# Optimization experiments

Measured on AMD Instinct MI355X. Metric: run time of the kernel, lower is better.

The kernel has to match this reference:

```python
import jax, jax.numpy as jnp
import numpy as np

NEG_SLOPE = 0.2  # PyG GATConv default leaky_relu slope
EPS = 1e-16


def layer_norm(x, g, b):
    mu = x.mean(-1, keepdims=True)
    var = ((x - mu) ** 2).mean(-1, keepdims=True)
    return (x - mu) * jax.lax.rsqrt(var + 1e-5) * g + b


def gat_conv(x, src, dst, n, W, a_src, a_dst, bias):
    # x: [N, C_in]; W: [C_in, H*C]; a_src/a_dst: [H, C]; concat=False -> mean over heads
    H, C = a_src.shape
    xh = (x @ W).reshape(n, H, C)                      # [N, H, C]
    s_src = jnp.einsum('nhc,hc->nh', xh, a_src)         # [N, H]
    s_dst = jnp.einsum('nhc,hc->nh', xh, a_dst)         # [N, H]
    e = jax.nn.leaky_relu(s_src[src] + s_dst[dst], NEG_SLOPE)  # [E, H]
    # segment softmax over incoming edges of each destination node
    m = jax.ops.segment_max(e, dst, num_segments=n)     # [N, H]
    ee = jnp.exp(e - m[dst])
    z = jax.ops.segment_sum(ee, dst, num_segments=n)    # [N, H]
    alpha = ee / (z[dst] + EPS)                         # [E, H]
    msg = xh[src] * alpha[:, :, None]                   # [E, H, C]
    out = jax.ops.segment_sum(msg, dst, num_segments=n) # [N, H, C]
    return out.mean(axis=1) + bias                      # [N, C]


def setup_inputs() -> dict:
    key = jax.random.key(0)
    N, E, C, H, L = 50000, 400000, 64, 4, 2
    ks = jax.random.split(key, 16)
    x = jax.random.normal(ks[0], (N, C), dtype=jnp.float32)
    edge_index = jax.random.randint(ks[1], (2, E), 0, N, dtype=jnp.int64)
    sc = 1.0 / np.sqrt(C)
    return {
        'x': x,
        'edge_index': edge_index,
        'Wg': jax.random.normal(ks[2], (L, C, H * C), dtype=jnp.float32) * sc,
        'att_src': jax.random.normal(ks[3], (L, H, C), dtype=jnp.float32) * sc,
        'att_dst': jax.random.normal(ks[4], (L, H, C), dtype=jnp.float32) * sc,
        'att_bias': jnp.zeros((L, C), dtype=jnp.float32),
        'ln1_g': jnp.ones((L, C), dtype=jnp.float32),
        'ln1_b': jnp.zeros((L, C), dtype=jnp.float32),
        'W1': jax.random.normal(ks[5], (L, C, C), dtype=jnp.float32) * sc,
        'b1': jnp.zeros((L, C), dtype=jnp.float32),
        'W2': jax.random.normal(ks[6], (L, C, C), dtype=jnp.float32) * sc,
        'b2': jnp.zeros((L, C), dtype=jnp.float32),
        'ln2_g': jnp.ones((L, C), dtype=jnp.float32),
        'ln2_b': jnp.zeros((L, C), dtype=jnp.float32),
    }


def reference(x, edge_index, Wg, att_src, att_dst, att_bias,
              ln1_g, ln1_b, W1, b1, W2, b2, ln2_g, ln2_b):
    n = x.shape[0]
    L = Wg.shape[0]
    # PyG GATConv adds self loops by default
    loops = jnp.arange(n, dtype=edge_index.dtype)
    src = jnp.concatenate([edge_index[0], loops])
    dst = jnp.concatenate([edge_index[1], loops])
    for i in range(L):
        x_att = gat_conv(x, src, dst, n, Wg[i], att_src[i], att_dst[i], att_bias[i])
        x = layer_norm(x + x_att, ln1_g[i], ln1_b[i])
        h = jax.nn.relu(x @ W1[i] + b1[i])
        h = h @ W2[i] + b2[i]
        x = layer_norm(x + h, ln2_g[i], ln2_b[i])
    return x
```

## Files before the change

kernel.cpp:

```cpp
#include <hip/hip_runtime.h>
#include <hip/hip_bf16.h>
#include <float.h>

#define C 64
#define H 4
#define HC 256
#define NEG_SLOPE 0.2f
#define EPS_SEG 1e-16f
#define LN_EPS 1e-5f

typedef __attribute__((ext_vector_type(8))) short bf16x8;
typedef __attribute__((ext_vector_type(4))) float f32x4;

__device__ __forceinline__ float warp_sum(float v) {
#pragma unroll
    for (int m = 32; m >= 1; m >>= 1) v += __shfl_xor(v, m, 64);
    return v;
}

__device__ __forceinline__ unsigned short f2bf(float f) {
    unsigned int u = __float_as_uint(f);
    return (unsigned short)((u + 0x7FFF + ((u >> 16) & 1)) >> 16);
}
__device__ __forceinline__ float bf2f(unsigned short u) {
    return __uint_as_float(((unsigned int)u) << 16);
}


__global__ void k_zero(int* __restrict__ a, int n) {
    int i = blockIdx.x * blockDim.x + threadIdx.x;
    int stride = gridDim.x * blockDim.x;
    for (int j = i; j < n; j += stride) a[j] = 0;
}

__global__ void k_count(const int* __restrict__ ei, int* __restrict__ counts,
                        int E, int Etot) {
    int eid = blockIdx.x * blockDim.x + threadIdx.x;
    if (eid >= Etot) return;
    int d = (eid < E) ? ei[E + eid] : eid - E;
    atomicAdd(&counts[d], 1);
}

__global__ __launch_bounds__(256) void k_scan1(const int* __restrict__ counts,
                                               int* __restrict__ tmp,
                                               int* __restrict__ bsum, int N) {
    __shared__ int sm[256];
    int t = threadIdx.x;
    int i = blockIdx.x * 256 + t;
    sm[t] = (i < N) ? counts[i] : 0;
    __syncthreads();
    for (int off = 1; off < 256; off <<= 1) {
        int add = (t >= off) ? sm[t - off] : 0;
        __syncthreads();
        sm[t] += add;
        __syncthreads();
    }
    if (i < N) tmp[i] = sm[t];
    if (t == 255) bsum[blockIdx.x] = sm[255];
}

__global__ __launch_bounds__(256) void k_scan2(int* __restrict__ bsum, int nb) {
    __shared__ int sm[256];
    int t = threadIdx.x;
    sm[t] = (t < nb) ? bsum[t] : 0;
    __syncthreads();
    for (int off = 1; off < 256; off <<= 1) {
        int add = (t >= off) ? sm[t - off] : 0;
        __syncthreads();
        sm[t] += add;
        __syncthreads();
    }
    if (t < nb) bsum[t] = (t > 0) ? sm[t - 1] : 0;
}

__global__ __launch_bounds__(256) void k_scan3(const int* __restrict__ tmp,
                                               const int* __restrict__ boff,
                                               int* __restrict__ rowptr,
                                               int* __restrict__ cursor, int N) {
    int i = blockIdx.x * 256 + threadIdx.x;
    if (i < N) {
        rowptr[i + 1] = tmp[i] + boff[blockIdx.x];
        cursor[i] = 0;
    }
    if (i == 0) rowptr[0] = 0;
}

__global__ void k_fill(const int* __restrict__ ei, const int* __restrict__ rowptr,
                       int* __restrict__ cursor, int* __restrict__ col,
                       int* __restrict__ dcol, int E, int Etot) {
    int eid = blockIdx.x * blockDim.x + threadIdx.x;
    if (eid >= Etot) return;
    int s, d;
    if (eid < E) { s = ei[eid]; d = ei[E + eid]; } else { s = d = eid - E; }
    int pos = rowptr[d] + atomicAdd(&cursor[d], 1);
    col[pos] = s;
    dcol[pos] = d;
}


__global__ void k_prep_x(const float4* __restrict__ xin, ushort4* __restrict__ xb,
                         int n4, int npad4) {
    int i = blockIdx.x * blockDim.x + threadIdx.x;
    int st = gridDim.x * blockDim.x;
    for (int j = i; j < npad4; j += st) {
        ushort4 o;
        if (j < n4) {
            float4 v = xin[j];
            o.x = f2bf(v.x); o.y = f2bf(v.y); o.z = f2bf(v.z); o.w = f2bf(v.w);
        } else {
            o.x = o.y = o.z = o.w = 0;
        }
        xb[j] = o;
    }
}

__global__ void k_prep_w(const float* __restrict__ Wg, unsigned short* __restrict__ Wgt,
                         int L) {
    int i = blockIdx.x * 256 + threadIdx.x;
    if (i < L * C * HC) {
        int l = i / (C * HC);
        int r = i - l * C * HC;
        int n = r >> 6, k = r & 63;
        Wgt[(size_t)l * HC * C + n * C + k] = f2bf(Wg[(size_t)l * C * HC + k * HC + n]);
    }
}

__global__ void k_prep_fw(const float* __restrict__ W1, const float* __restrict__ W2,
                          unsigned short* __restrict__ W1t, unsigned short* __restrict__ W2t,
                          int L) {
    int i = blockIdx.x * 256 + threadIdx.x;
    if (i < L * C * C) {
        int l = i / (C * C);
        int r = i - l * C * C;
        int n = r >> 6, k = r & 63;
        W1t[(size_t)l * C * C + n * C + k] = f2bf(W1[(size_t)l * C * C + k * C + n]);
        W2t[(size_t)l * C * C + n * C + k] = f2bf(W2[(size_t)l * C * C + k * C + n]);
    }
}

__global__ __launch_bounds__(256) void k_gemm_mfma(
    const unsigned short* __restrict__ xb, const unsigned short* __restrict__ Wgt,
    const float* __restrict__ a_src, const float* __restrict__ a_dst,
    unsigned short* __restrict__ xh, float* __restrict__ s_src,
    float* __restrict__ s_dst, int N)
{
    int w = threadIdx.x >> 6, l = threadIdx.x & 63;
    int n0 = blockIdx.x * 64;
    int lr = l & 15, lk = (l >> 4) * 8;
    bf16x8 bfr[4][2];
    float as[4], ad[4];
#pragma unroll
    for (int ct = 0; ct < 4; ct++) {
        int colg = w * 64 + ct * 16 + lr;
#pragma unroll
        for (int ks = 0; ks < 2; ks++)
            bfr[ct][ks] = *reinterpret_cast<const bf16x8*>(Wgt + colg * C + ks * 32 + lk);
        as[ct] = a_src[w * C + ct * 16 + lr];
        ad[ct] = a_dst[w * C + ct * 16 + lr];
    }
#pragma unroll
    for (int rt = 0; rt < 4; rt++) {
        const unsigned short* arow = xb + (size_t)(n0 + rt * 16 + lr) * C + lk;
        bf16x8 a0 = *reinterpret_cast<const bf16x8*>(arow);
        bf16x8 a1 = *reinterpret_cast<const bf16x8*>(arow + 32);
        f32x4 acc[4];
#pragma unroll
        for (int ct = 0; ct < 4; ct++) {
            acc[ct] = (f32x4){0.f, 0.f, 0.f, 0.f};
            acc[ct] = __builtin_amdgcn_mfma_f32_16x16x32_bf16(a0, bfr[ct][0], acc[ct], 0, 0, 0);
            acc[ct] = __builtin_amdgcn_mfma_f32_16x16x32_bf16(a1, bfr[ct][1], acc[ct], 0, 0, 0);
        }
        int nbase = n0 + rt * 16 + (l >> 4) * 4;
#pragma unroll
        for (int ct = 0; ct < 4; ct++) {
            int colg = w * 64 + ct * 16 + lr;
#pragma unroll
            for (int r = 0; r < 4; r++) {
                int n = nbase + r;
                if (n < N) xh[(size_t)n * HC + colg] = f2bf(acc[ct][r]);
            }
        }
#pragma unroll
        for (int r = 0; r < 4; r++) {
            float ps = acc[0][r] * as[0] + acc[1][r] * as[1]
                     + acc[2][r] * as[2] + acc[3][r] * as[3];
            float pd = acc[0][r] * ad[0] + acc[1][r] * ad[1]
                     + acc[2][r] * ad[2] + acc[3][r] * ad[3];
#pragma unroll
            for (int off = 1; off < 16; off <<= 1) {
                ps += __shfl_xor(ps, off, 64);
                pd += __shfl_xor(pd, off, 64);
            }
            int n = nbase + r;
            if (lr == 0 && n < N) {
                s_src[n * H + w] = ps;
                s_dst[n * H + w] = pd;
            }
        }
    }
}

__global__ void k_edge_w(const int* __restrict__ col, const int* __restrict__ dcol,
                         const float* __restrict__ s_src, const float* __restrict__ s_dst,
                         float* __restrict__ wbuf, int Etot) {
    int i = blockIdx.x * blockDim.x + threadIdx.x;
    if (i >= Etot * H) return;
    int p = i >> 2, h = i & 3;
    int s = col[p], d = dcol[p];
    float e = s_src[s * H + h] + s_dst[d * H + h];
    e = e >= 0.f ? e : NEG_SLOPE * e;
    wbuf[i] = __expf(e);
}

__global__ __launch_bounds__(256) void k_gat_node(
    const int* __restrict__ rowptr, const int* __restrict__ col,
    const float* __restrict__ wbuf, const unsigned short* __restrict__ xh,
    const float* __restrict__ x_in, const float* __restrict__ bias,
    const float* __restrict__ g, const float* __restrict__ b,
    float* __restrict__ x1, unsigned short* __restrict__ x1b, int N)
{
    int n = (blockIdx.x * blockDim.x + threadIdx.x) >> 6;
    int l = threadIdx.x & 63;
    int h = l >> 4, gq = l & 15;
    if (n >= N) return;
    int r0 = rowptr[n], r1 = rowptr[n + 1];

    float4 xi = *(const float4*)(x_in + (size_t)n * C + gq * 4);
    float4 bia = *(const float4*)(bias + gq * 4);

    const char* xbase = (const char*)xh;
    int laneoff = h * 128 + gq * 8;

    float a0 = 0.f, a1 = 0.f, a2 = 0.f, a3 = 0.f, z = 0.f;

    int j = r0;
    for (; j + 4 <= r1; j += 4) {
        int s0 = col[j], s1 = col[j + 1], s2 = col[j + 2], s3 = col[j + 3];
        float w0 = wbuf[(j + 0) * H + h];
        float w1 = wbuf[(j + 1) * H + h];
        float w2 = wbuf[(j + 2) * H + h];
        float w3 = wbuf[(j + 3) * H + h];
        uint2 v0 = *(const uint2*)(xbase + (size_t)s0 * 512 + laneoff);
        uint2 v1 = *(const uint2*)(xbase + (size_t)s1 * 512 + laneoff);
        uint2 v2 = *(const uint2*)(xbase + (size_t)s2 * 512 + laneoff);
        uint2 v3 = *(const uint2*)(xbase + (size_t)s3 * 512 + laneoff);
        a0 += w0 * __uint_as_float(v0.x << 16);
        a1 += w0 * __uint_as_float(v0.x & 0xFFFF0000u);
        a2 += w0 * __uint_as_float(v0.y << 16);
        a3 += w0 * __uint_as_float(v0.y & 0xFFFF0000u);
        a0 += w1 * __uint_as_float(v1.x << 16);
        a1 += w1 * __uint_as_float(v1.x & 0xFFFF0000u);
        a2 += w1 * __uint_as_float(v1.y << 16);
        a3 += w1 * __uint_as_float(v1.y & 0xFFFF0000u);
        a0 += w2 * __uint_as_float(v2.x << 16);
        a1 += w2 * __uint_as_float(v2.x & 0xFFFF0000u);
        a2 += w2 * __uint_as_float(v2.y << 16);
        a3 += w2 * __uint_as_float(v2.y & 0xFFFF0000u);
        a0 += w3 * __uint_as_float(v3.x << 16);
        a1 += w3 * __uint_as_float(v3.x & 0xFFFF0000u);
        a2 += w3 * __uint_as_float(v3.y << 16);
        a3 += w3 * __uint_as_float(v3.y & 0xFFFF0000u);
        z += w0 + w1 + w2 + w3;
    }
    {
        int t = r1 - j;
        int s0 = 0, s1 = 0, s2 = 0;
        float w0 = 0.f, w1 = 0.f, w2 = 0.f;
        if (t > 0) { s0 = col[j];     w0 = wbuf[(j + 0) * H + h]; }
        if (t > 1) { s1 = col[j + 1]; w1 = wbuf[(j + 1) * H + h]; }
        if (t > 2) { s2 = col[j + 2]; w2 = wbuf[(j + 2) * H + h]; }
        uint2 v0 = {0, 0}, v1 = {0, 0}, v2 = {0, 0};
        if (t > 0) v0 = *(const uint2*)(xbase + (size_t)s0 * 512 + laneoff);
        if (t > 1) v1 = *(const uint2*)(xbase + (size_t)s1 * 512 + laneoff);
        if (t > 2) v2 = *(const uint2*)(xbase + (size_t)s2 * 512 + laneoff);
        a0 += w0 * __uint_as_float(v0.x << 16);
        a1 += w0 * __uint_as_float(v0.x & 0xFFFF0000u);
        a2 += w0 * __uint_as_float(v0.y << 16);
        a3 += w0 * __uint_as_float(v0.y & 0xFFFF0000u);
        a0 += w1 * __uint_as_float(v1.x << 16);
        a1 += w1 * __uint_as_float(v1.x & 0xFFFF0000u);
        a2 += w1 * __uint_as_float(v1.y << 16);
        a3 += w1 * __uint_as_float(v1.y & 0xFFFF0000u);
        a0 += w2 * __uint_as_float(v2.x << 16);
        a1 += w2 * __uint_as_float(v2.x & 0xFFFF0000u);
        a2 += w2 * __uint_as_float(v2.y << 16);
        a3 += w2 * __uint_as_float(v2.y & 0xFFFF0000u);
        z += w0 + w1 + w2;
    }

    float inv = 0.25f / (z + EPS_SEG);
    a0 *= inv; a1 *= inv; a2 *= inv; a3 *= inv;
#pragma unroll
    for (int off = 16; off <= 32; off <<= 1) {
        a0 += __shfl_xor(a0, off, 64);
        a1 += __shfl_xor(a1, off, 64);
        a2 += __shfl_xor(a2, off, 64);
        a3 += __shfl_xor(a3, off, 64);
    }
    float y0 = xi.x + a0 + bia.x;
    float y1 = xi.y + a1 + bia.y;
    float y2 = xi.z + a2 + bia.z;
    float y3 = xi.w + a3 + bia.w;
    float mu = warp_sum(y0 + y1 + y2 + y3) * (1.f / (C * 4));
    float d0 = y0 - mu, d1 = y1 - mu, d2 = y2 - mu, d3 = y3 - mu;
    float var = warp_sum(d0 * d0 + d1 * d1 + d2 * d2 + d3 * d3) * (1.f / (C * 4));
    float rs = rsqrtf(var + LN_EPS);
    if (h == 0) {
        float4 gg = *(const float4*)(g + gq * 4);
        float4 bb = *(const float4*)(b + gq * 4);
        float4 o;
        o.x = d0 * rs * gg.x + bb.x;
        o.y = d1 * rs * gg.y + bb.y;
        o.z = d2 * rs * gg.z + bb.z;
        o.w = d3 * rs * gg.w + bb.w;
        *(float4*)(x1 + (size_t)n * C + gq * 4) = o;
        ushort4 ob;
        ob.x = f2bf(o.x); ob.y = f2bf(o.y); ob.z = f2bf(o.z); ob.w = f2bf(o.w);
        *(ushort4*)(x1b + (size_t)n * C + gq * 4) = ob;
    }
}

__global__ __launch_bounds__(256) void k_ffn_mfma(
    const float* __restrict__ x1f, const unsigned short* __restrict__ x1b,
    const unsigned short* __restrict__ W1t, const unsigned short* __restrict__ W2t,
    const float* __restrict__ b1, const float* __restrict__ b2,
    const float* __restrict__ g, const float* __restrict__ b,
    float* __restrict__ xout, unsigned short* __restrict__ xb, int N)
{
    __shared__ unsigned short hls[64 * 64];
    int w = threadIdx.x >> 6, l = threadIdx.x & 63;
    int lr = l & 15, q = l >> 4, lk = q * 8;
    int n0 = blockIdx.x * 64;

    {
        bf16x8 bf[4][2];
#pragma unroll
        for (int ct = 0; ct < 4; ct++)
#pragma unroll
            for (int ks = 0; ks < 2; ks++)
                bf[ct][ks] = *reinterpret_cast<const bf16x8*>(
                    W1t + (ct * 16 + lr) * C + ks * 32 + lk);
        const unsigned short* arow = x1b + (size_t)(n0 + w * 16 + lr) * C + lk;
        bf16x8 a0 = *reinterpret_cast<const bf16x8*>(arow);
        bf16x8 a1 = *reinterpret_cast<const bf16x8*>(arow + 32);
        f32x4 acc[4];
#pragma unroll
        for (int ct = 0; ct < 4; ct++) {
            acc[ct] = (f32x4){0.f, 0.f, 0.f, 0.f};
            acc[ct] = __builtin_amdgcn_mfma_f32_16x16x32_bf16(a0, bf[ct][0], acc[ct], 0, 0, 0);
            acc[ct] = __builtin_amdgcn_mfma_f32_16x16x32_bf16(a1, bf[ct][1], acc[ct], 0, 0, 0);
        }
#pragma unroll
        for (int ct = 0; ct < 4; ct++) {
            float bc = b1[ct * 16 + lr];
#pragma unroll
            for (int r = 0; r < 4; r++) {
                float v = fmaxf(acc[ct][r] + bc, 0.f);
                int rowb = w * 16 + q * 4 + r;
                int byte = rowb * 128 + (ct * 16 + lr) * 2;
                byte ^= (rowb & 7) << 4;
                *(unsigned short*)((char*)hls + byte) = f2bf(v);
            }
        }
    }
    __syncthreads();

    bf16x8 bf[4][2];
#pragma unroll
    for (int ct = 0; ct < 4; ct++)
#pragma unroll
        for (int ks = 0; ks < 2; ks++)
            bf[ct][ks] = *reinterpret_cast<const bf16x8*>(
                W2t + (ct * 16 + lr) * C + ks * 32 + lk);
    bf16x8 h0, h1;
    {
        int rowb = w * 16 + lr;
        int swz = (rowb & 7) << 4;
        int byte0 = (rowb * 128 + q * 16) ^ swz;
        int byte1 = (rowb * 128 + 64 + q * 16) ^ swz;
        h0 = *(bf16x8*)((char*)hls + byte0);
        h1 = *(bf16x8*)((char*)hls + byte1);
    }
    f32x4 acc[4];
#pragma unroll
    for (int ct = 0; ct < 4; ct++) {
        acc[ct] = (f32x4){0.f, 0.f, 0.f, 0.f};
        acc[ct] = __builtin_amdgcn_mfma_f32_16x16x32_bf16(h0, bf[ct][0], acc[ct], 0, 0, 0);
        acc[ct] = __builtin_amdgcn_mfma_f32_16x16x32_bf16(h1, bf[ct][1], acc[ct], 0, 0, 0);
    }

    float b2c[4], gc[4], bc[4];
#pragma unroll
    for (int ct = 0; ct < 4; ct++) {
        int cg = ct * 16 + lr;
        b2c[ct] = b2[cg]; gc[ct] = g[cg]; bc[ct] = b[cg];
    }
    float yv[4][4];
#pragma unroll
    for (int r = 0; r < 4; r++) {
        int n = n0 + w * 16 + q * 4 + r;
        bool ok = n < N;
#pragma unroll
        for (int ct = 0; ct < 4; ct++) {
            float xr = ok ? x1f[(size_t)n * C + ct * 16 + lr] : 0.f;
            yv[ct][r] = acc[ct][r] + b2c[ct] + xr;
        }
    }
#pragma unroll
    for (int r = 0; r < 4; r++) {
        int n = n0 + w * 16 + q * 4 + r;
        float s = yv[0][r] + yv[1][r] + yv[2][r] + yv[3][r];
#pragma unroll
        for (int off = 1; off < 16; off <<= 1) s += __shfl_xor(s, off, 64);
        float mu = s * (1.f / C);
        float d0 = yv[0][r] - mu, d1 = yv[1][r] - mu;
        float d2 = yv[2][r] - mu, d3 = yv[3][r] - mu;
        float vs = d0 * d0 + d1 * d1 + d2 * d2 + d3 * d3;
#pragma unroll
        for (int off = 1; off < 16; off <<= 1) vs += __shfl_xor(vs, off, 64);
        float rs = rsqrtf(vs * (1.f / C) + LN_EPS);
        if (n < N) {
            float dd[4] = {d0, d1, d2, d3};
#pragma unroll
            for (int ct = 0; ct < 4; ct++) {
                float o = dd[ct] * rs * gc[ct] + bc[ct];
                xout[(size_t)n * C + ct * 16 + lr] = o;
                xb[(size_t)n * C + ct * 16 + lr] = f2bf(o);
            }
        }
    }
}

extern "C" void kernel_launch(void* const* d_in, const int* in_sizes, int n_in,
                              void* d_out, int out_size, void* d_ws, size_t ws_size,
                              hipStream_t stream) {
    const float* x        = (const float*)d_in[0];
    const int*   ei       = (const int*)d_in[1];
    const float* Wg       = (const float*)d_in[2];
    const float* a_src    = (const float*)d_in[3];
    const float* a_dst    = (const float*)d_in[4];
    const float* att_bias = (const float*)d_in[5];
    const float* ln1_g    = (const float*)d_in[6];
    const float* ln1_b    = (const float*)d_in[7];
    const float* W1       = (const float*)d_in[8];
    const float* b1       = (const float*)d_in[9];
    const float* W2       = (const float*)d_in[10];
    const float* b2       = (const float*)d_in[11];
    const float* ln2_g    = (const float*)d_in[12];
    const float* ln2_b    = (const float*)d_in[13];
    float* xout = (float*)d_out;

    int N = in_sizes[0] / C;
    int E = in_sizes[1] / 2;
    int Etot = E + N;
    int L = in_sizes[2] / (C * HC);
    int nb = (N + 255) / 256;
    int Npad = (N + 63) & ~63;

    char* p = (char*)d_ws;
    auto alloc = [&](size_t bytes) { void* r = (void*)p; p += (bytes + 255) & ~(size_t)255; return r; };
    float* s_src = (float*)alloc((size_t)N * H * 4);
    float* s_dst = (float*)alloc((size_t)N * H * 4);
    float* x1    = (float*)alloc((size_t)N * C * 4);
    float* wbuf  = (float*)alloc((size_t)Etot * H * 4);
    int* rowptr  = (int*)alloc((size_t)(N + 1) * 4);
    int* col     = (int*)alloc((size_t)Etot * 4);
    int* dcol    = (int*)alloc((size_t)Etot * 4);
    int* counts  = (int*)alloc((size_t)N * 4);
    int* tmp     = (int*)alloc((size_t)N * 4);
    int* bsum    = (int*)alloc((size_t)nb * 4);
    unsigned short* xb  = (unsigned short*)alloc((size_t)Npad * C * 2);
    unsigned short* x1b = (unsigned short*)alloc((size_t)Npad * C * 2);
    unsigned short* Wgt = (unsigned short*)alloc((size_t)L * HC * C * 2);
    unsigned short* W1t = (unsigned short*)alloc((size_t)L * C * C * 2);
    unsigned short* W2t = (unsigned short*)alloc((size_t)L * C * C * 2);
    unsigned short* xh  = (unsigned short*)alloc((size_t)N * HC * 2);

    k_zero<<<256, 256, 0, stream>>>(counts, N);
    k_count<<<(Etot + 255) / 256, 256, 0, stream>>>(ei, counts, E, Etot);
    k_scan1<<<nb, 256, 0, stream>>>(counts, tmp, bsum, N);
    k_scan2<<<1, 256, 0, stream>>>(bsum, nb);
    k_scan3<<<nb, 256, 0, stream>>>(tmp, bsum, rowptr, counts, N);
    k_fill<<<(Etot + 255) / 256, 256, 0, stream>>>(ei, rowptr, counts, col, dcol, E, Etot);
    k_prep_x<<<2048, 256, 0, stream>>>((const float4*)x, (ushort4*)xb,
                                       N * C / 4, Npad * C / 4);
    k_prep_w<<<(2 * C * HC + 255) / 256, 256, 0, stream>>>(Wg, Wgt, L);
    k_prep_fw<<<(2 * C * C + 255) / 256, 256, 0, stream>>>(W1, W2, W1t, W2t, L);

    for (int l = 0; l < L; l++) {
        const float* xin = (l == 0) ? x : xout;
        k_gemm_mfma<<<Npad / 64, 256, 0, stream>>>(
            xb, Wgt + (size_t)l * HC * C, a_src + l * H * C, a_dst + l * H * C,
            xh, s_src, s_dst, N);
        k_edge_w<<<(Etot * H + 255) / 256, 256, 0, stream>>>(
            col, dcol, s_src, s_dst, wbuf, Etot);
        k_gat_node<<<(N + 3) / 4, 256, 0, stream>>>(
            rowptr, col, wbuf, xh, xin,
            att_bias + l * C, ln1_g + l * C, ln1_b + l * C, x1, x1b, N);
        k_ffn_mfma<<<Npad / 64, 256, 0, stream>>>(
            x1, x1b, W1t + (size_t)l * C * C, W2t + (size_t)l * C * C,
            b1 + l * C, b2 + l * C, ln2_g + l * C, ln2_b + l * C, xout, xb, N);
    }
}
```

Measured before the change: 232.0 us.

## Split each node's edge gather across two wavefronts and combine via LDS

The GAT aggregation kernel now assigns two wavefronts per destination node, each handling alternating edges (stride 2), then combines partial sums and normalizer through shared memory before the layer-norm epilogue. This aims to double memory-level parallelism on the latency-bound gather of source features for nodes with about 9 incoming edges. It doubles the number of blocks, adds a block-wide barrier and LDS traffic, and leaves half the wavefronts idle during the epilogue.

```diff
diff --git a/kernel.cpp b/kernel.cpp
--- a/kernel.cpp
+++ b/kernel.cpp
@@ -219,27 +219,35 @@
     const float* __restrict__ g, const float* __restrict__ b,
     float* __restrict__ x1, unsigned short* __restrict__ x1b, int N)
 {
-    int n = (blockIdx.x * blockDim.x + threadIdx.x) >> 6;
+    __shared__ float part[2][64][5];
+    int w = threadIdx.x >> 6;
     int l = threadIdx.x & 63;
     int h = l >> 4, gq = l & 15;
-    if (n >= N) return;
-    int r0 = rowptr[n], r1 = rowptr[n + 1];
-
-    float4 xi = *(const float4*)(x_in + (size_t)n * C + gq * 4);
-    float4 bia = *(const float4*)(bias + gq * 4);
+    int nl = w >> 1;
+    int half = w & 1;
+    int n = blockIdx.x * 2 + nl;
+    bool valid = n < N;
+    int r0 = 0, r1 = 0;
+    if (valid) { r0 = rowptr[n]; r1 = rowptr[n + 1]; }
+
+    float4 xi = {0.f, 0.f, 0.f, 0.f}, bia = {0.f, 0.f, 0.f, 0.f};
+    if (valid && half == 0) {
+        xi = *(const float4*)(x_in + (size_t)n * C + gq * 4);
+        bia = *(const float4*)(bias + gq * 4);
+    }
 
     const char* xbase = (const char*)xh;
     int laneoff = h * 128 + gq * 8;
 
     float a0 = 0.f, a1 = 0.f, a2 = 0.f, a3 = 0.f, z = 0.f;
 
-    int j = r0;
-    for (; j + 4 <= r1; j += 4) {
-        int s0 = col[j], s1 = col[j + 1], s2 = col[j + 2], s3 = col[j + 3];
+    int j = r0 + half;
+    for (; j + 6 < r1; j += 8) {
+        int s0 = col[j], s1 = col[j + 2], s2 = col[j + 4], s3 = col[j + 6];
         float w0 = wbuf[(j + 0) * H + h];
-        float w1 = wbuf[(j + 1) * H + h];
-        float w2 = wbuf[(j + 2) * H + h];
-        float w3 = wbuf[(j + 3) * H + h];
+        float w1 = wbuf[(j + 2) * H + h];
+        float w2 = wbuf[(j + 4) * H + h];
+        float w3 = wbuf[(j + 6) * H + h];
         uint2 v0 = *(const uint2*)(xbase + (size_t)s0 * 512 + laneoff);
         uint2 v1 = *(const uint2*)(xbase + (size_t)s1 * 512 + laneoff);
         uint2 v2 = *(const uint2*)(xbase + (size_t)s2 * 512 + laneoff);
@@ -263,16 +271,15 @@
         z += w0 + w1 + w2 + w3;
     }
     {
-        int t = r1 - j;
         int s0 = 0, s1 = 0, s2 = 0;
         float w0 = 0.f, w1 = 0.f, w2 = 0.f;
-        if (t > 0) { s0 = col[j];     w0 = wbuf[(j + 0) * H + h]; }
-        if (t > 1) { s1 = col[j + 1]; w1 = wbuf[(j + 1) * H + h]; }
-        if (t > 2) { s2 = col[j + 2]; w2 = wbuf[(j + 2) * H + h]; }
+        if (j < r1)     { s0 = col[j];     w0 = wbuf[(j + 0) * H + h]; }
+        if (j + 2 < r1) { s1 = col[j + 2]; w1 = wbuf[(j + 2) * H + h]; }
+        if (j + 4 < r1) { s2 = col[j + 4]; w2 = wbuf[(j + 4) * H + h]; }
         uint2 v0 = {0, 0}, v1 = {0, 0}, v2 = {0, 0};
-        if (t > 0) v0 = *(const uint2*)(xbase + (size_t)s0 * 512 + laneoff);
-        if (t > 1) v1 = *(const uint2*)(xbase + (size_t)s1 * 512 + laneoff);
-        if (t > 2) v2 = *(const uint2*)(xbase + (size_t)s2 * 512 + laneoff);
+        if (j < r1)     v0 = *(const uint2*)(xbase + (size_t)s0 * 512 + laneoff);
+        if (j + 2 < r1) v1 = *(const uint2*)(xbase + (size_t)s1 * 512 + laneoff);
+        if (j + 4 < r1) v2 = *(const uint2*)(xbase + (size_t)s2 * 512 + laneoff);
         a0 += w0 * __uint_as_float(v0.x << 16);
         a1 += w0 * __uint_as_float(v0.x & 0xFFFF0000u);
         a2 += w0 * __uint_as_float(v0.y << 16);
@@ -287,6 +294,16 @@
         a3 += w2 * __uint_as_float(v2.y & 0xFFFF0000u);
         z += w0 + w1 + w2;
     }
+
+    if (half == 1) {
+        part[nl][l][0] = a0; part[nl][l][1] = a1; part[nl][l][2] = a2;
+        part[nl][l][3] = a3; part[nl][l][4] = z;
+    }
+    __syncthreads();
+    if (half != 0) return;
+    a0 += part[nl][l][0]; a1 += part[nl][l][1]; a2 += part[nl][l][2];
+    a3 += part[nl][l][3]; z  += part[nl][l][4];
+    if (!valid) return;
 
     float inv = 0.25f / (z + EPS_SEG);
     a0 *= inv; a1 *= inv; a2 *= inv; a3 *= inv;
@@ -494,7 +511,7 @@
             xh, s_src, s_dst, N);
         k_edge_w<<<(Etot * H + 255) / 256, 256, 0, stream>>>(
             col, dcol, s_src, s_dst, wbuf, Etot);
-        k_gat_node<<<(N + 3) / 4, 256, 0, stream>>>(
+        k_gat_node<<<(N + 1) / 2, 256, 0, stream>>>(
             rowptr, col, wbuf, xh, xin,
             att_bias + l * C, ln1_g + l * C, ln1_b + l * C, x1, x1b, N);
         k_ffn_mfma<<<Npad / 64, 256, 0, stream>>>(
```

Measured after the change: 242.5 us. +4.5%, slower.

## Fuse edge-weight computation into node aggregation and pack s_src beside features

Applied to the files above, without the earlier changes.

Drops the separate per-edge weight kernel and its wbuf/dcol buffers. The aggregation kernel now computes exp(leaky_relu(s_src+s_dst)) inline, reading s_src from a 576-byte padded row that also holds the bf16 features of the source node, so one row fetch supplies both. Weight prep kernels are also merged into one launch. The cost is recomputing the exp per lane in the gather loop and a wider, less aligned row stride for the gathered features.

```diff
diff --git a/kernel.cpp b/kernel.cpp
--- a/kernel.cpp
+++ b/kernel.cpp
@@ -8,6 +8,7 @@
 #define NEG_SLOPE 0.2f
 #define EPS_SEG 1e-16f
 #define LN_EPS 1e-5f
+#define ROWB 576
 
 typedef __attribute__((ext_vector_type(8))) short bf16x8;
 typedef __attribute__((ext_vector_type(4))) float f32x4;
@@ -87,14 +88,13 @@
 
 __global__ void k_fill(const int* __restrict__ ei, const int* __restrict__ rowptr,
                        int* __restrict__ cursor, int* __restrict__ col,
-                       int* __restrict__ dcol, int E, int Etot) {
+                       int E, int Etot) {
     int eid = blockIdx.x * blockDim.x + threadIdx.x;
     if (eid >= Etot) return;
     int s, d;
     if (eid < E) { s = ei[eid]; d = ei[E + eid]; } else { s = d = eid - E; }
     int pos = rowptr[d] + atomicAdd(&cursor[d], 1);
     col[pos] = s;
-    dcol[pos] = d;
 }
 
 
@@ -114,24 +114,23 @@
     }
 }
 
-__global__ void k_prep_w(const float* __restrict__ Wg, unsigned short* __restrict__ Wgt,
-                         int L) {
+__global__ void k_prep_weights(const float* __restrict__ Wg,
+                               const float* __restrict__ W1, const float* __restrict__ W2,
+                               unsigned short* __restrict__ Wgt,
+                               unsigned short* __restrict__ W1t,
+                               unsigned short* __restrict__ W2t, int L) {
     int i = blockIdx.x * 256 + threadIdx.x;
-    if (i < L * C * HC) {
+    int nWg = L * C * HC;
+    int nW = L * C * C;
+    if (i < nWg) {
         int l = i / (C * HC);
         int r = i - l * C * HC;
         int n = r >> 6, k = r & 63;
         Wgt[(size_t)l * HC * C + n * C + k] = f2bf(Wg[(size_t)l * C * HC + k * HC + n]);
-    }
-}
-
-__global__ void k_prep_fw(const float* __restrict__ W1, const float* __restrict__ W2,
-                          unsigned short* __restrict__ W1t, unsigned short* __restrict__ W2t,
-                          int L) {
-    int i = blockIdx.x * 256 + threadIdx.x;
-    if (i < L * C * C) {
-        int l = i / (C * C);
-        int r = i - l * C * C;
+    } else if (i < nWg + nW) {
+        int j = i - nWg;
+        int l = j / (C * C);
+        int r = j - l * C * C;
         int n = r >> 6, k = r & 63;
         W1t[(size_t)l * C * C + n * C + k] = f2bf(W1[(size_t)l * C * C + k * C + n]);
         W2t[(size_t)l * C * C + n * C + k] = f2bf(W2[(size_t)l * C * C + k * C + n]);
@@ -141,8 +140,7 @@
 __global__ __launch_bounds__(256) void k_gemm_mfma(
     const unsigned short* __restrict__ xb, const unsigned short* __restrict__ Wgt,
     const float* __restrict__ a_src, const float* __restrict__ a_dst,
-    unsigned short* __restrict__ xh, float* __restrict__ s_src,
-    float* __restrict__ s_dst, int N)
+    char* __restrict__ xhs, float* __restrict__ s_dst, int N)
 {
     int w = threadIdx.x >> 6, l = threadIdx.x & 63;
     int n0 = blockIdx.x * 64;
@@ -173,11 +171,12 @@
         int nbase = n0 + rt * 16 + (l >> 4) * 4;
 #pragma unroll
         for (int ct = 0; ct < 4; ct++) {
-            int colg = w * 64 + ct * 16 + lr;
+            int cb = (w * 64 + ct * 16 + lr) * 2;
 #pragma unroll
             for (int r = 0; r < 4; r++) {
                 int n = nbase + r;
-                if (n < N) xh[(size_t)n * HC + colg] = f2bf(acc[ct][r]);
+                if (n < N)
+                    *(unsigned short*)(xhs + (size_t)n * ROWB + cb) = f2bf(acc[ct][r]);
             }
         }
 #pragma unroll
@@ -193,28 +192,16 @@
             }
             int n = nbase + r;
             if (lr == 0 && n < N) {
-                s_src[n * H + w] = ps;
+                *(float*)(xhs + (size_t)n * ROWB + 512 + w * 4) = ps;
                 s_dst[n * H + w] = pd;
             }
         }
     }
 }
 
-__global__ void k_edge_w(const int* __restrict__ col, const int* __restrict__ dcol,
-                         const float* __restrict__ s_src, const float* __restrict__ s_dst,
-                         float* __restrict__ wbuf, int Etot) {
-    int i = blockIdx.x * blockDim.x + threadIdx.x;
-    if (i >= Etot * H) return;
-    int p = i >> 2, h = i & 3;
-    int s = col[p], d = dcol[p];
-    float e = s_src[s * H + h] + s_dst[d * H + h];
-    e = e >= 0.f ? e : NEG_SLOPE * e;
-    wbuf[i] = __expf(e);
-}
-
 __global__ __launch_bounds__(256) void k_gat_node(
     const int* __restrict__ rowptr, const int* __restrict__ col,
-    const float* __restrict__ wbuf, const unsigned short* __restrict__ xh,
+    const float* __restrict__ s_dst, const char* __restrict__ xhs,
     const float* __restrict__ x_in, const float* __restrict__ bias,
     const float* __restrict__ g, const float* __restrict__ b,
     float* __restrict__ x1, unsigned short* __restrict__ x1b, int N)
@@ -227,23 +214,32 @@
 
     float4 xi = *(const float4*)(x_in + (size_t)n * C + gq * 4);
     float4 bia = *(const float4*)(bias + gq * 4);
-
-    const char* xbase = (const char*)xh;
+    float sdh = s_dst[n * H + h];
+
     int laneoff = h * 128 + gq * 8;
+    int ssoff = 512 + h * 4;
 
     float a0 = 0.f, a1 = 0.f, a2 = 0.f, a3 = 0.f, z = 0.f;
 
     int j = r0;
     for (; j + 4 <= r1; j += 4) {
         int s0 = col[j], s1 = col[j + 1], s2 = col[j + 2], s3 = col[j + 3];
-        float w0 = wbuf[(j + 0) * H + h];
-        float w1 = wbuf[(j + 1) * H + h];
-        float w2 = wbuf[(j + 2) * H + h];
-        float w3 = wbuf[(j + 3) * H + h];
-        uint2 v0 = *(const uint2*)(xbase + (size_t)s0 * 512 + laneoff);
-        uint2 v1 = *(const uint2*)(xbase + (size_t)s1 * 512 + laneoff);
-        uint2 v2 = *(const uint2*)(xbase + (size_t)s2 * 512 + laneoff);
-        uint2 v3 = *(const uint2*)(xbase + (size_t)s3 * 512 + laneoff);
+        const char* p0 = xhs + (size_t)s0 * ROWB;
+        const char* p1 = xhs + (size_t)s1 * ROWB;
+        const char* p2 = xhs + (size_t)s2 * ROWB;
+        const char* p3 = xhs + (size_t)s3 * ROWB;
+        uint2 v0 = *(const uint2*)(p0 + laneoff);
+        uint2 v1 = *(const uint2*)(p1 + laneoff);
+        uint2 v2 = *(const uint2*)(p2 + laneoff);
+        uint2 v3 = *(const uint2*)(p3 + laneoff);
+        float e0 = *(const float*)(p0 + ssoff) + sdh;
+        float e1 = *(const float*)(p1 + ssoff) + sdh;
+        float e2 = *(const float*)(p2 + ssoff) + sdh;
+        float e3 = *(const float*)(p3 + ssoff) + sdh;
+        float w0 = __expf(fmaxf(e0, NEG_SLOPE * e0));
+        float w1 = __expf(fmaxf(e1, NEG_SLOPE * e1));
+        float w2 = __expf(fmaxf(e2, NEG_SLOPE * e2));
+        float w3 = __expf(fmaxf(e3, NEG_SLOPE * e3));
         a0 += w0 * __uint_as_float(v0.x << 16);
         a1 += w0 * __uint_as_float(v0.x & 0xFFFF0000u);
         a2 += w0 * __uint_as_float(v0.y << 16);
@@ -265,14 +261,20 @@
     {
         int t = r1 - j;
         int s0 = 0, s1 = 0, s2 = 0;
-        float w0 = 0.f, w1 = 0.f, w2 = 0.f;
-        if (t > 0) { s0 = col[j];     w0 = wbuf[(j + 0) * H + h]; }
-        if (t > 1) { s1 = col[j + 1]; w1 = wbuf[(j + 1) * H + h]; }
-        if (t > 2) { s2 = col[j + 2]; w2 = wbuf[(j + 2) * H + h]; }
+        if (t > 0) s0 = col[j];
+        if (t > 1) s1 = col[j + 1];
+        if (t > 2) s2 = col[j + 2];
+        const char* p0 = xhs + (size_t)s0 * ROWB;
+        const char* p1 = xhs + (size_t)s1 * ROWB;
+        const char* p2 = xhs + (size_t)s2 * ROWB;
         uint2 v0 = {0, 0}, v1 = {0, 0}, v2 = {0, 0};
-        if (t > 0) v0 = *(const uint2*)(xbase + (size_t)s0 * 512 + laneoff);
-        if (t > 1) v1 = *(const uint2*)(xbase + (size_t)s1 * 512 + laneoff);
-        if (t > 2) v2 = *(const uint2*)(xbase + (size_t)s2 * 512 + laneoff);
+        float e0 = 0.f, e1 = 0.f, e2 = 0.f;
+        if (t > 0) { v0 = *(const uint2*)(p0 + laneoff); e0 = *(const float*)(p0 + ssoff) + sdh; }
+        if (t > 1) { v1 = *(const uint2*)(p1 + laneoff); e1 = *(const float*)(p1 + ssoff) + sdh; }
+        if (t > 2) { v2 = *(const uint2*)(p2 + laneoff); e2 = *(const float*)(p2 + ssoff) + sdh; }
+        float w0 = (t > 0) ? __expf(fmaxf(e0, NEG_SLOPE * e0)) : 0.f;
+        float w1 = (t > 1) ? __expf(fmaxf(e1, NEG_SLOPE * e1)) : 0.f;
+        float w2 = (t > 2) ? __expf(fmaxf(e2, NEG_SLOPE * e2)) : 0.f;
         a0 += w0 * __uint_as_float(v0.x << 16);
         a1 += w0 * __uint_as_float(v0.x & 0xFFFF0000u);
         a2 += w0 * __uint_as_float(v0.y << 16);
@@ -459,13 +461,10 @@
 
     char* p = (char*)d_ws;
     auto alloc = [&](size_t bytes) { void* r = (void*)p; p += (bytes + 255) & ~(size_t)255; return r; };
-    float* s_src = (float*)alloc((size_t)N * H * 4);
     float* s_dst = (float*)alloc((size_t)N * H * 4);
     float* x1    = (float*)alloc((size_t)N * C * 4);
-    float* wbuf  = (float*)alloc((size_t)Etot * H * 4);
     int* rowptr  = (int*)alloc((size_t)(N + 1) * 4);
     int* col     = (int*)alloc((size_t)Etot * 4);
-    int* dcol    = (int*)alloc((size_t)Etot * 4);
     int* counts  = (int*)alloc((size_t)N * 4);
     int* tmp     = (int*)alloc((size_t)N * 4);
     int* bsum    = (int*)alloc((size_t)nb * 4);
@@ -474,28 +473,28 @@
     unsigned short* Wgt = (unsigned short*)alloc((size_t)L * HC * C * 2);
     unsigned short* W1t = (unsigned short*)alloc((size_t)L * C * C * 2);
     unsigned short* W2t = (unsigned short*)alloc((size_t)L * C * C * 2);
-    unsigned short* xh  = (unsigned short*)alloc((size_t)N * HC * 2);
+    char* xhs = (char*)alloc((size_t)N * ROWB);
 
     k_zero<<<256, 256, 0, stream>>>(counts, N);
     k_count<<<(Etot + 255) / 256, 256, 0, stream>>>(ei, counts, E, Etot);
     k_scan1<<<nb, 256, 0, stream>>>(counts, tmp, bsum, N);
     k_scan2<<<1, 256, 0, stream>>>(bsum, nb);
     k_scan3<<<nb, 256, 0, stream>>>(tmp, bsum, rowptr, counts, N);
-    k_fill<<<(Etot + 255) / 256, 256, 0, stream>>>(ei, rowptr, counts, col, dcol, E, Etot);
+    k_fill<<<(Etot + 255) / 256, 256, 0, stream>>>(ei, rowptr, counts, col, E, Etot);
     k_prep_x<<<2048, 256, 0, stream>>>((const float4*)x, (ushort4*)xb,
                                        N * C / 4, Npad * C / 4);
-    k_prep_w<<<(2 * C * HC + 255) / 256, 256, 0, stream>>>(Wg, Wgt, L);
-    k_prep_fw<<<(2 * C * C + 255) / 256, 256, 0, stream>>>(W1, W2, W1t, W2t, L);
+    {
+        int tot = L * C * HC + L * C * C;
+        k_prep_weights<<<(tot + 255) / 256, 256, 0, stream>>>(Wg, W1, W2, Wgt, W1t, W2t, L);
+    }
 
     for (int l = 0; l < L; l++) {
         const float* xin = (l == 0) ? x : xout;
         k_gemm_mfma<<<Npad / 64, 256, 0, stream>>>(
             xb, Wgt + (size_t)l * HC * C, a_src + l * H * C, a_dst + l * H * C,
-            xh, s_src, s_dst, N);
-        k_edge_w<<<(Etot * H + 255) / 256, 256, 0, stream>>>(
-            col, dcol, s_src, s_dst, wbuf, Etot);
+            xhs, s_dst, N);
         k_gat_node<<<(N + 3) / 4, 256, 0, stream>>>(
-            rowptr, col, wbuf, xh, xin,
+            rowptr, col, s_dst, xhs, xin,
             att_bias + l * C, ln1_g + l * C, ln1_b + l * C, x1, x1b, N);
         k_ffn_mfma<<<Npad / 64, 256, 0, stream>>>(
             x1, x1b, W1t + (size_t)l * C * C, W2t + (size_t)l * C * C,
```

Result: faster. 218.5 us (-5.8%).
